# Optimization experiments

Measured on AMD Instinct MI355X. Metric: run time of the kernel, lower is better.

The kernel has to match this reference:

```python
import math
import jax, jax.numpy as jnp
import numpy as np

N = 512
C_S, C_Z, C_H, H, PQ, PV = 384, 128, 16, 12, 4, 8
INF, EPS = 1e5, 1e-8


def _quat_to_rot(q):
    # q: [N,4] unnormalized quaternions -> [N,3,3] rotation matrices
    q = q / jnp.linalg.norm(q, axis=-1, keepdims=True)
    w, x, y, z = q[:, 0], q[:, 1], q[:, 2], q[:, 3]
    return jnp.stack([
        jnp.stack([1 - 2 * (y * y + z * z), 2 * (x * y - w * z), 2 * (x * z + w * y)], -1),
        jnp.stack([2 * (x * y + w * z), 1 - 2 * (x * x + z * z), 2 * (y * z - w * x)], -1),
        jnp.stack([2 * (x * z - w * y), 2 * (y * z + w * x), 1 - 2 * (x * x + y * y)], -1),
    ], -2)


def setup_inputs() -> dict:
    key = jax.random.key(0)
    ks = jax.random.split(key, 16)
    sc = 0.02
    inp = {
        "s": jax.random.normal(ks[0], (N, C_S), jnp.float32),
        "z": jax.random.normal(ks[1], (N, N, C_Z), jnp.float32),
        "rot": _quat_to_rot(jax.random.normal(ks[2], (N, 4), jnp.float32)),
        "trans": jax.random.normal(ks[3], (N, 3), jnp.float32) * 10.0,
        "mask": jnp.ones((N,), jnp.float32),
        "Wq": jax.random.normal(ks[4], (C_S, H * C_H), jnp.float32) * sc,
        "bq": jnp.zeros((H * C_H,), jnp.float32),
        "Wkv": jax.random.normal(ks[5], (C_S, 2 * H * C_H), jnp.float32) * sc,
        "bkv": jnp.zeros((2 * H * C_H,), jnp.float32),
        "Wqp": jax.random.normal(ks[6], (C_S, H * 3 * PQ), jnp.float32) * sc,
        "bqp": jnp.zeros((H * 3 * PQ,), jnp.float32),
        "Wkvp": jax.random.normal(ks[7], (C_S, H * 3 * (PQ + PV)), jnp.float32) * sc,
        "bkvp": jnp.zeros((H * 3 * (PQ + PV),), jnp.float32),
        "Wb": jax.random.normal(ks[8], (C_Z, H), jnp.float32) * sc,
        "bb": jnp.zeros((H,), jnp.float32),
        "head_weights": jnp.full((H,), math.log(math.e - 1.0), jnp.float32),
        "Wout": jax.random.normal(ks[9], (H * (C_Z + C_H + PV * 4), C_S), jnp.float32) * sc,
        "bout": jnp.zeros((C_S,), jnp.float32),
    }
    return inp


def _ipa(s, z, rot, trans, mask, Wq, bq, Wkv, bkv, Wqp, bqp, Wkvp, bkvp, Wb, bb, head_weights, Wout, bout):
    q = (s @ Wq + bq).reshape(N, H, C_H)
    kv = (s @ Wkv + bkv).reshape(N, H, 2 * C_H)
    k, v = kv[..., :C_H], kv[..., C_H:]

    def proj_pts(W, b, P):
        # torch: split last dim into 3 chunks, stack on -1 -> layout [N, 3, H, P] -> [N, H, P, 3]
        pl = (s @ W + b).reshape(N, 3, H, P).transpose(0, 2, 3, 1)
        return jnp.einsum('nij,nhpj->nhpi', rot, pl) + trans[:, None, None, :]

    q_pts = proj_pts(Wqp, bqp, PQ)                    # [N,H,PQ,3]
    kv_pts = proj_pts(Wkvp, bkvp, PQ + PV)            # [N,H,PQ+PV,3]
    k_pts, v_pts = kv_pts[..., :PQ, :], kv_pts[..., PQ:, :]

    b_bias = z @ Wb + bb                              # [N,N,H]
    a = jnp.einsum('ihc,jhc->hij', q, k) * math.sqrt(1.0 / (3 * C_H))
    a = a + math.sqrt(1.0 / 3) * b_bias.transpose(2, 0, 1)

    d2 = jnp.sum((q_pts[:, None] - k_pts[None]) ** 2, axis=-1)   # [i,j,H,PQ]
    hw = jax.nn.softplus(head_weights) * math.sqrt(1.0 / (3 * (PQ * 9.0 / 2)))
    pt_att = -0.5 * jnp.sum(d2 * hw[None, None, :, None], axis=-1)  # [i,j,H]

    sq_mask = INF * (mask[:, None] * mask[None, :] - 1.0)
    a = jax.nn.softmax(a + pt_att.transpose(2, 0, 1) + sq_mask[None], axis=-1)  # [H,i,j]

    o = jnp.einsum('hij,jhc->ihc', a, v).reshape(N, H * C_H)
    o_pt = jnp.einsum('hij,jhpc->ihpc', a, v_pts)                 # [i,H,PV,3]
    o_pt = jnp.einsum('nji,nhpj->nhpi', rot, o_pt - trans[:, None, None, :])  # invert_apply
    o_pt_norm = jnp.sqrt(jnp.sum(o_pt ** 2, axis=-1) + EPS).reshape(N, H * PV)
    o_pt_flat = o_pt.reshape(N, H * PV, 3)
    o_pair = jnp.einsum('hij,ijc->ihc', a, z).reshape(N, H * C_Z)

    cat = jnp.concatenate(
        [o, o_pt_flat[..., 0], o_pt_flat[..., 1], o_pt_flat[..., 2], o_pt_norm, o_pair], axis=-1)
    return cat @ Wout + bout


def reference(s, z, rot, trans, mask, Wq, bq, Wkv, bkv, Wqp, bqp, Wkvp, bkvp, Wb, bb, head_weights, Wout, bout):
    return _ipa(s, z, rot, trans, mask, Wq, bq, Wkv, bkv, Wqp, bqp, Wkvp, bkvp, Wb, bb, head_weights, Wout, bout)
```

## Files before the change

kernel.cpp:

```cpp
#include <hip/hip_runtime.h>
#include <math.h>

#define NN 512
#define CS 384
#define CZ 128
#define CH 16
#define HH 12
#define PQ 4
#define PV 8
#define LGS_S 516

typedef float f32x4 __attribute__((ext_vector_type(4)));
typedef __bf16 bf16x8 __attribute__((ext_vector_type(8)));

__global__ void k_repack(const float* __restrict__ Wq,  const float* __restrict__ bq,
                         const float* __restrict__ Wkv, const float* __restrict__ bkv,
                         const float* __restrict__ Wqp, const float* __restrict__ bqp,
                         const float* __restrict__ Wkvp,const float* __restrict__ bkvp,
                         float* __restrict__ Wcat, float* __restrict__ bcat)
{
    const int total = CS * 1152;
    for (int idx = blockIdx.x * blockDim.x + threadIdx.x; idx < total; idx += gridDim.x * blockDim.x) {
        int kk = idx / 1152, n = idx % 1152;
        float vv;
        if (n < 192)      vv = Wq  [kk * 192 + n];
        else if (n < 576) vv = Wkv [kk * 384 + (n - 192)];
        else if (n < 720) vv = Wqp [kk * 144 + (n - 576)];
        else              vv = Wkvp[kk * 432 + (n - 720)];
        Wcat[idx] = vv;
    }
    int n = blockIdx.x * blockDim.x + threadIdx.x;
    if (n < 1152) {
        float vv;
        if (n < 192)      vv = bq  [n];
        else if (n < 576) vv = bkv [n - 192];
        else if (n < 720) vv = bqp [n - 576];
        else              vv = bkvp[n - 720];
        bcat[n] = vv;
    }
}

__global__ void k_proj(const float* __restrict__ s, const float* __restrict__ Wcat,
                       const float* __restrict__ bcat,
                       float* __restrict__ q, float* __restrict__ k_t, float* __restrict__ v,
                       float* __restrict__ qp_raw, float* __restrict__ kvp_raw)
{
    __shared__ float As[16 * 68];
    __shared__ float Bs[64 * 64];

    int tx = threadIdx.x & 15;
    int ty = threadIdx.x >> 4;
    int n0 = blockIdx.x * 64;
    int m0 = blockIdx.y * 16;

    float acc[4] = {0.f, 0.f, 0.f, 0.f};

    for (int kb = 0; kb < CS; kb += 64) {
        #pragma unroll
        for (int e = 0; e < 4; ++e) {
            int idx = e * 256 + threadIdx.x;
            int m = idx >> 6, kk = idx & 63;
            As[m * 68 + kk] = s[(size_t)(m0 + m) * CS + kb + kk];
        }
        #pragma unroll
        for (int e = 0; e < 16; ++e) {
            int idx = e * 256 + threadIdx.x;
            int kk = idx >> 6, n = idx & 63;
            Bs[kk * 64 + n] = Wcat[(size_t)(kb + kk) * 1152 + n0 + n];
        }
        __syncthreads();

        for (int kk = 0; kk < 64; kk += 4) {
            f32x4 a = *(const f32x4*)&As[ty * 68 + kk];
            f32x4 b[4];
            #pragma unroll
            for (int kq = 0; kq < 4; ++kq)
                b[kq] = *(const f32x4*)&Bs[(kk + kq) * 64 + tx * 4];
            #pragma unroll
            for (int kq = 0; kq < 4; ++kq)
                #pragma unroll
                for (int cc = 0; cc < 4; ++cc)
                    acc[cc] += a[kq] * b[kq][cc];
        }
        __syncthreads();
    }

    int i = m0 + ty;
    #pragma unroll
    for (int cc = 0; cc < 4; ++cc) {
        int col = n0 + tx * 4 + cc;
        float val = acc[cc] + bcat[col];
        if (col < 192) {
            q[i * 192 + col] = val;
        } else if (col < 576) {
            int lc = col - 192;
            int h = lc / 32, w = lc % 32;
            if (w < CH) k_t[(h * CH + w) * NN + i] = val;
            else        v[(i * HH + h) * CH + (w - CH)] = val;
        } else if (col < 720) {
            qp_raw[i * 144 + (col - 576)] = val;
        } else {
            kvp_raw[i * 432 + (col - 720)] = val;
        }
    }
}

__global__ void k_pts_transform(const float* __restrict__ qp_raw, const float* __restrict__ kvp_raw,
                                const float* __restrict__ rot, const float* __restrict__ trans,
                                float* __restrict__ q_pts, float* __restrict__ k_pts_t,
                                float* __restrict__ v_pts)
{
    int idx = blockIdx.x * blockDim.x + threadIdx.x;
    const int total = NN * HH * 16;
    if (idx >= total) return;
    int i = idx / (HH * 16);
    int r = idx % (HH * 16);
    int h = r / 16;
    int p = r % 16;

    float R[9], t3[3];
    for (int a = 0; a < 9; ++a) R[a] = rot[i * 9 + a];
    for (int a = 0; a < 3; ++a) t3[a] = trans[i * 3 + a];

    float x, y, zc;
    if (p < PQ) {
        x  = qp_raw[i * 144 + 0 * 48 + h * PQ + p];
        y  = qp_raw[i * 144 + 1 * 48 + h * PQ + p];
        zc = qp_raw[i * 144 + 2 * 48 + h * PQ + p];
    } else {
        int pp = p - PQ;
        x  = kvp_raw[i * 432 + 0 * 144 + h * 12 + pp];
        y  = kvp_raw[i * 432 + 1 * 144 + h * 12 + pp];
        zc = kvp_raw[i * 432 + 2 * 144 + h * 12 + pp];
    }
    float ox = R[0] * x + R[1] * y + R[2] * zc + t3[0];
    float oy = R[3] * x + R[4] * y + R[5] * zc + t3[1];
    float oz = R[6] * x + R[7] * y + R[8] * zc + t3[2];

    if (p < PQ) {
        int o = ((i * HH + h) * PQ + p) * 3;
        q_pts[o] = ox; q_pts[o + 1] = oy; q_pts[o + 2] = oz;
    } else {
        int pp = p - PQ;
        if (pp < PQ) {
            int rb = (h * PQ + pp) * 3;
            k_pts_t[(size_t)(rb + 0) * NN + i] = ox;
            k_pts_t[(size_t)(rb + 1) * NN + i] = oy;
            k_pts_t[(size_t)(rb + 2) * NN + i] = oz;
        } else {
            int o = ((i * HH + h) * PV + (pp - PQ)) * 3;
            v_pts[o] = ox; v_pts[o + 1] = oy; v_pts[o + 2] = oz;
        }
    }
}

__global__ void __launch_bounds__(512, 4)
k_attn(const float* __restrict__ z, const float* __restrict__ Wb,
       const float* __restrict__ bb,
       const float* __restrict__ q, const float* __restrict__ k_t,
       const float* __restrict__ q_pts, const float* __restrict__ k_pts_t,
       const float* __restrict__ head_weights, const float* __restrict__ mask,
       const float* __restrict__ v, const float* __restrict__ v_pts,
       const float* __restrict__ rot, const float* __restrict__ trans,
       float* __restrict__ cat)
{
    __shared__ float lgs[HH][LGS_S];
    __shared__ float q_lds[HH * CH];
    __shared__ float qp_lds[HH * PQ * 3];
    __shared__ float hw_lds[HH];
    __shared__ float bb_l[HH];
    __shared__ float opt_lds[HH * PV * 3];

    const int i = blockIdx.x;
    const int tid = threadIdx.x;
    const int lane = tid & 63;
    const int wave = tid >> 6;
    const float* zbase = z + (size_t)i * NN * CZ;

    if (tid < HH * CH)     q_lds[tid]  = q[(size_t)i * HH * CH + tid];
    if (tid < HH * PQ * 3) qp_lds[tid] = q_pts[(size_t)i * HH * PQ * 3 + tid];
    if (tid < HH) {
        float x = head_weights[tid];
        hw_lds[tid] = log1pf(expf(x)) * 0.13608276348795434f;
        bb_l[tid] = bb[tid];
    }

    {
        const float b_scale = 0.57735026918962576f;
        const int hcol = lane & 15;
        const int q8 = (lane >> 4) * 8;
        bf16x8 wbf[4];
        #pragma unroll
        for (int kc = 0; kc < 4; ++kc) {
            #pragma unroll
            for (int jj = 0; jj < 8; ++jj) {
                int c = kc * 32 + q8 + jj;
                float wv = (hcol < HH) ? Wb[c * HH + hcol] * b_scale : 0.0f;
                wbf[kc][jj] = (__bf16)wv;
            }
        }
        #pragma unroll
        for (int t = 0; t < 4; ++t) {
            int j0 = (wave * 4 + t) * 16;
            const float* zrow = zbase + (size_t)(j0 + hcol) * CZ;
            f32x4 acc = {0.f, 0.f, 0.f, 0.f};
            #pragma unroll
            for (int kc = 0; kc < 4; ++kc) {
                float4 z0 = *(const float4*)(zrow + kc * 32 + q8);
                float4 z1 = *(const float4*)(zrow + kc * 32 + q8 + 4);
                bf16x8 afrag;
                afrag[0] = (__bf16)z0.x; afrag[1] = (__bf16)z0.y;
                afrag[2] = (__bf16)z0.z; afrag[3] = (__bf16)z0.w;
                afrag[4] = (__bf16)z1.x; afrag[5] = (__bf16)z1.y;
                afrag[6] = (__bf16)z1.z; afrag[7] = (__bf16)z1.w;
                acc = __builtin_amdgcn_mfma_f32_16x16x32_bf16(afrag, wbf[kc], acc, 0, 0, 0);
            }
            if (hcol < HH) {
                #pragma unroll
                for (int r = 0; r < 4; ++r) {
                    int j = j0 + (lane >> 4) * 4 + r;
                    lgs[hcol][j] = acc[r];
                }
            }
        }
    }
    __syncthreads();

    {
        const float qk_scale = 0.14433756729740643f;
        const float b_scale  = 0.57735026918962576f;
        const float sqm = 100000.0f * (mask[i] * mask[tid] - 1.0f);
        #pragma unroll
        for (int h = 0; h < HH; ++h) {
            float accq = 0.f;
            #pragma unroll
            for (int c = 0; c < CH; ++c)
                accq += q_lds[h * CH + c] * k_t[(size_t)(h * CH + c) * NN + tid];
            float s2 = 0.f;
            #pragma unroll
            for (int p = 0; p < PQ; ++p) {
                int rb = (h * PQ + p) * 3;
                float dx = qp_lds[rb + 0] - k_pts_t[(size_t)(rb + 0) * NN + tid];
                float dy = qp_lds[rb + 1] - k_pts_t[(size_t)(rb + 1) * NN + tid];
                float dz = qp_lds[rb + 2] - k_pts_t[(size_t)(rb + 2) * NN + tid];
                s2 += dx * dx + dy * dy + dz * dz;
            }
            lgs[h][tid] += accq * qk_scale + b_scale * bb_l[h] - 0.5f * hw_lds[h] * s2 + sqm;
        }
    }
    __syncthreads();

    for (int row = wave; row < HH; row += 8) {
        float vals[8];
        float m = -1e30f;
        #pragma unroll
        for (int u = 0; u < 8; ++u) { vals[u] = lgs[row][lane + u * 64]; m = fmaxf(m, vals[u]); }
        #pragma unroll
        for (int off = 32; off >= 1; off >>= 1) m = fmaxf(m, __shfl_xor(m, off));
        float ssum = 0.f;
        #pragma unroll
        for (int u = 0; u < 8; ++u) { vals[u] = expf(vals[u] - m); ssum += vals[u]; }
        #pragma unroll
        for (int off = 32; off >= 1; off >>= 1) ssum += __shfl_xor(ssum, off);
        float inv = 1.0f / ssum;
        #pragma unroll
        for (int u = 0; u < 8; ++u) lgs[row][lane + u * 64] = vals[u] * inv;
    }
    __syncthreads();

    if (tid < 480) {
        float acc = 0.f;
        if (tid < 192) {
            const float* lr = lgs[tid >> 4];
            const float* vp = v + tid;
            #pragma unroll 4
            for (int j = 0; j < NN; ++j)
                acc += lr[j] * vp[(size_t)j * 192];
            cat[(size_t)i * 2112 + tid] = acc;
        } else {
            int r = tid - 192;
            const float* lr = lgs[r / 24];
            const float* vp = v_pts + r;
            #pragma unroll 4
            for (int j = 0; j < NN; ++j)
                acc += lr[j] * vp[(size_t)j * 288];
            opt_lds[r] = acc;
        }
    }

    {
        int cl = lane & 15;
        int q4 = lane >> 4;
        int ha = (cl < HH) ? cl : (HH - 1);
        int cb = wave * 16 + cl;
        f32x4 pacc = {0.f, 0.f, 0.f, 0.f};
        for (int ks = 0; ks < 16; ++ks) {
            int jb = ks * 32 + q4 * 8;
            f32x4 a0 = *(const f32x4*)&lgs[ha][jb];
            f32x4 a1 = *(const f32x4*)&lgs[ha][jb + 4];
            bf16x8 af;
            af[0] = (__bf16)a0[0]; af[1] = (__bf16)a0[1];
            af[2] = (__bf16)a0[2]; af[3] = (__bf16)a0[3];
            af[4] = (__bf16)a1[0]; af[5] = (__bf16)a1[1];
            af[6] = (__bf16)a1[2]; af[7] = (__bf16)a1[3];
            bf16x8 bf;
            #pragma unroll
            for (int jj = 0; jj < 8; ++jj)
                bf[jj] = (__bf16)zbase[(size_t)(jb + jj) * CZ + cb];
            pacc = __builtin_amdgcn_mfma_f32_16x16x32_bf16(af, bf, pacc, 0, 0, 0);
        }
        float* crow = cat + (size_t)i * 2112 + 576;
        #pragma unroll
        for (int r = 0; r < 4; ++r) {
            int h = q4 * 4 + r;
            if (h < HH) crow[h * CZ + cb] = pacc[r];
        }
    }
    __syncthreads();

    if (tid < HH * PV) {
        int hp = tid;
        float R[9], t3[3];
        #pragma unroll
        for (int a2 = 0; a2 < 9; ++a2) R[a2] = rot[i * 9 + a2];
        #pragma unroll
        for (int a2 = 0; a2 < 3; ++a2) t3[a2] = trans[i * 3 + a2];
        float gx = opt_lds[hp * 3 + 0] - t3[0];
        float gy = opt_lds[hp * 3 + 1] - t3[1];
        float gz = opt_lds[hp * 3 + 2] - t3[2];
        float lx = R[0] * gx + R[3] * gy + R[6] * gz;
        float ly = R[1] * gx + R[4] * gy + R[7] * gz;
        float lz = R[2] * gx + R[5] * gy + R[8] * gz;
        float* crow = cat + (size_t)i * 2112;
        crow[192 + 0 * 96 + hp] = lx;
        crow[192 + 1 * 96 + hp] = ly;
        crow[192 + 2 * 96 + hp] = lz;
        crow[480 + hp] = sqrtf(lx * lx + ly * ly + lz * lz + 1e-8f);
    }
}

__global__ void k_final(const float* __restrict__ cat, const float* __restrict__ Wout,
                        const float* __restrict__ bout, float* __restrict__ out)
{
    __shared__ float As[16 * 52];
    __shared__ float Bs[48 * 64];

    int tx = threadIdx.x & 15;
    int ty = threadIdx.x >> 4;
    int n0 = blockIdx.x * 64;
    int m0 = blockIdx.y * 16;
    int k0 = blockIdx.z * 528;

    float acc[4] = {0.f, 0.f, 0.f, 0.f};

    for (int stage = 0; stage < 11; ++stage) {
        int kb = k0 + stage * 48;
        #pragma unroll
        for (int e = 0; e < 3; ++e) {
            int idx = e * 256 + threadIdx.x;
            int m = idx / 48, kk = idx % 48;
            As[m * 52 + kk] = cat[(size_t)(m0 + m) * 2112 + kb + kk];
        }
        #pragma unroll
        for (int e = 0; e < 12; ++e) {
            int idx = e * 256 + threadIdx.x;
            int kk = idx >> 6, n = idx & 63;
            Bs[kk * 64 + n] = Wout[(size_t)(kb + kk) * 384 + n0 + n];
        }
        __syncthreads();

        for (int kk = 0; kk < 48; kk += 4) {
            f32x4 a = *(const f32x4*)&As[ty * 52 + kk];
            f32x4 b[4];
            #pragma unroll
            for (int kq = 0; kq < 4; ++kq)
                b[kq] = *(const f32x4*)&Bs[(kk + kq) * 64 + tx * 4];
            #pragma unroll
            for (int kq = 0; kq < 4; ++kq)
                #pragma unroll
                for (int cc = 0; cc < 4; ++cc)
                    acc[cc] += a[kq] * b[kq][cc];
        }
        __syncthreads();
    }

    bool add_bias = (blockIdx.z == 0);
    int m = m0 + ty;
    #pragma unroll
    for (int cc = 0; cc < 4; ++cc) {
        int n = n0 + tx * 4 + cc;
        float val = acc[cc] + (add_bias ? bout[n] : 0.f);
        atomicAdd(&out[(size_t)m * 384 + n], val);
    }
}

extern "C" void kernel_launch(void* const* d_in, const int* in_sizes, int n_in,
                              void* d_out, int out_size, void* d_ws, size_t ws_size,
                              hipStream_t stream)
{
    const float* s     = (const float*)d_in[0];
    const float* z     = (const float*)d_in[1];
    const float* rot   = (const float*)d_in[2];
    const float* trans = (const float*)d_in[3];
    const float* mask  = (const float*)d_in[4];
    const float* Wq    = (const float*)d_in[5];
    const float* bq    = (const float*)d_in[6];
    const float* Wkv   = (const float*)d_in[7];
    const float* bkv   = (const float*)d_in[8];
    const float* Wqp   = (const float*)d_in[9];
    const float* bqp   = (const float*)d_in[10];
    const float* Wkvp  = (const float*)d_in[11];
    const float* bkvp  = (const float*)d_in[12];
    const float* Wb    = (const float*)d_in[13];
    const float* bb    = (const float*)d_in[14];
    const float* hw    = (const float*)d_in[15];
    const float* Wout  = (const float*)d_in[16];
    const float* bout  = (const float*)d_in[17];
    float* out = (float*)d_out;

    float* ws = (float*)d_ws;
    float* q       = ws;
    float* k_t     = ws + 98304;
    float* v       = ws + 196608;
    float* qp_raw  = ws + 294912;
    float* kvp_raw = ws + 368640;
    float* q_pts   = ws + 589824;
    float* k_pts_t = ws + 663552;
    float* v_pts   = ws + 737280;
    float* cat     = ws + 884736;
    float* Wcat    = ws + 1966080;
    float* bcat    = ws + 2408448;

    hipMemsetAsync(out, 0, (size_t)NN * CS * sizeof(float), stream);

    hipLaunchKernelGGL(k_repack, dim3(512), dim3(256), 0, stream,
                       Wq, bq, Wkv, bkv, Wqp, bqp, Wkvp, bkvp, Wcat, bcat);
    hipLaunchKernelGGL(k_proj, dim3(18, 32), dim3(256), 0, stream,
                       s, Wcat, bcat, q, k_t, v, qp_raw, kvp_raw);
    hipLaunchKernelGGL(k_pts_transform, dim3(384), dim3(256), 0, stream,
                       qp_raw, kvp_raw, rot, trans, q_pts, k_pts_t, v_pts);
    hipLaunchKernelGGL(k_attn, dim3(NN), dim3(512), 0, stream,
                       z, Wb, bb, q, k_t, q_pts, k_pts_t, hw, mask,
                       v, v_pts, rot, trans, cat);
    hipLaunchKernelGGL(k_final, dim3(6, 32, 4), dim3(256), 0, stream, cat, Wout, bout, out);
}
```

Baseline: 349.4 us.

## Drop weight repack kernel, hoist logit loads, and split pair-MFMA over K halves

```diff
diff --git a/kernel.cpp b/kernel.cpp
--- a/kernel.cpp
+++ b/kernel.cpp
@@ -13,35 +13,11 @@
 typedef float f32x4 __attribute__((ext_vector_type(4)));
 typedef __bf16 bf16x8 __attribute__((ext_vector_type(8)));
 
-__global__ void k_repack(const float* __restrict__ Wq,  const float* __restrict__ bq,
-                         const float* __restrict__ Wkv, const float* __restrict__ bkv,
-                         const float* __restrict__ Wqp, const float* __restrict__ bqp,
-                         const float* __restrict__ Wkvp,const float* __restrict__ bkvp,
-                         float* __restrict__ Wcat, float* __restrict__ bcat)
-{
-    const int total = CS * 1152;
-    for (int idx = blockIdx.x * blockDim.x + threadIdx.x; idx < total; idx += gridDim.x * blockDim.x) {
-        int kk = idx / 1152, n = idx % 1152;
-        float vv;
-        if (n < 192)      vv = Wq  [kk * 192 + n];
-        else if (n < 576) vv = Wkv [kk * 384 + (n - 192)];
-        else if (n < 720) vv = Wqp [kk * 144 + (n - 576)];
-        else              vv = Wkvp[kk * 432 + (n - 720)];
-        Wcat[idx] = vv;
-    }
-    int n = blockIdx.x * blockDim.x + threadIdx.x;
-    if (n < 1152) {
-        float vv;
-        if (n < 192)      vv = bq  [n];
-        else if (n < 576) vv = bkv [n - 192];
-        else if (n < 720) vv = bqp [n - 576];
-        else              vv = bkvp[n - 720];
-        bcat[n] = vv;
-    }
-}
-
-__global__ void k_proj(const float* __restrict__ s, const float* __restrict__ Wcat,
-                       const float* __restrict__ bcat,
+__global__ void k_proj(const float* __restrict__ s,
+                       const float* __restrict__ Wq,  const float* __restrict__ bq,
+                       const float* __restrict__ Wkv, const float* __restrict__ bkv,
+                       const float* __restrict__ Wqp, const float* __restrict__ bqp,
+                       const float* __restrict__ Wkvp,const float* __restrict__ bkvp,
                        float* __restrict__ q, float* __restrict__ k_t, float* __restrict__ v,
                        float* __restrict__ qp_raw, float* __restrict__ kvp_raw)
 {
@@ -66,7 +42,14 @@
         for (int e = 0; e < 16; ++e) {
             int idx = e * 256 + threadIdx.x;
             int kk = idx >> 6, n = idx & 63;
-            Bs[kk * 64 + n] = Wcat[(size_t)(kb + kk) * 1152 + n0 + n];
+            int col = n0 + n;
+            int kg = kb + kk;
+            float wv;
+            if (col < 192)      wv = Wq  [kg * 192 + col];
+            else if (col < 576) wv = Wkv [kg * 384 + (col - 192)];
+            else if (col < 720) wv = Wqp [kg * 144 + (col - 576)];
+            else                wv = Wkvp[kg * 432 + (col - 720)];
+            Bs[kk * 64 + n] = wv;
         }
         __syncthreads();
 
@@ -89,7 +72,12 @@
     #pragma unroll
     for (int cc = 0; cc < 4; ++cc) {
         int col = n0 + tx * 4 + cc;
-        float val = acc[cc] + bcat[col];
+        float bval;
+        if (col < 192)      bval = bq  [col];
+        else if (col < 576) bval = bkv [col - 192];
+        else if (col < 720) bval = bqp [col - 576];
+        else                bval = bkvp[col - 720];
+        float val = acc[cc] + bval;
         if (col < 192) {
             q[i * 192 + col] = val;
         } else if (col < 576) {
@@ -170,6 +158,7 @@
     __shared__ float hw_lds[HH];
     __shared__ float bb_l[HH];
     __shared__ float opt_lds[HH * PV * 3];
+    __shared__ float pair_lds[HH * CZ];
 
     const int i = blockIdx.x;
     const int tid = threadIdx.x;
@@ -183,6 +172,31 @@
         float x = head_weights[tid];
         hw_lds[tid] = log1pf(expf(x)) * 0.13608276348795434f;
         bb_l[tid] = bb[tid];
+    }
+    __syncthreads();
+
+    float lg[HH];
+    {
+        const float qk_scale = 0.14433756729740643f;
+        const float b_scale  = 0.57735026918962576f;
+        const float sqm = 100000.0f * (mask[i] * mask[tid] - 1.0f);
+        #pragma unroll
+        for (int h = 0; h < HH; ++h) {
+            float accq = 0.f;
+            #pragma unroll
+            for (int c = 0; c < CH; ++c)
+                accq += q_lds[h * CH + c] * k_t[(size_t)(h * CH + c) * NN + tid];
+            float s2 = 0.f;
+            #pragma unroll
+            for (int p = 0; p < PQ; ++p) {
+                int rb = (h * PQ + p) * 3;
+                float dx = qp_lds[rb + 0] - k_pts_t[(size_t)(rb + 0) * NN + tid];
+                float dy = qp_lds[rb + 1] - k_pts_t[(size_t)(rb + 1) * NN + tid];
+                float dz = qp_lds[rb + 2] - k_pts_t[(size_t)(rb + 2) * NN + tid];
+                s2 += dx * dx + dy * dy + dz * dz;
+            }
+            lg[h] = accq * qk_scale + b_scale * bb_l[h] - 0.5f * hw_lds[h] * s2 + sqm;
+        }
     }
 
     {
@@ -224,30 +238,14 @@
             }
         }
     }
-    __syncthreads();
-
-    {
-        const float qk_scale = 0.14433756729740643f;
-        const float b_scale  = 0.57735026918962576f;
-        const float sqm = 100000.0f * (mask[i] * mask[tid] - 1.0f);
-        #pragma unroll
-        for (int h = 0; h < HH; ++h) {
-            float accq = 0.f;
-            #pragma unroll
-            for (int c = 0; c < CH; ++c)
-                accq += q_lds[h * CH + c] * k_t[(size_t)(h * CH + c) * NN + tid];
-            float s2 = 0.f;
-            #pragma unroll
-            for (int p = 0; p < PQ; ++p) {
-                int rb = (h * PQ + p) * 3;
-                float dx = qp_lds[rb + 0] - k_pts_t[(size_t)(rb + 0) * NN + tid];
-                float dy = qp_lds[rb + 1] - k_pts_t[(size_t)(rb + 1) * NN + tid];
-                float dz = qp_lds[rb + 2] - k_pts_t[(size_t)(rb + 2) * NN + tid];
-                s2 += dx * dx + dy * dy + dz * dz;
-            }
-            lgs[h][tid] += accq * qk_scale + b_scale * bb_l[h] - 0.5f * hw_lds[h] * s2 + sqm;
-        }
-    }
+
+    asm volatile("s_waitcnt lgkmcnt(0)" ::: "memory");
+    __builtin_amdgcn_sched_barrier(0);
+
+    #pragma unroll
+    for (int h = 0; h < HH; ++h)
+        lgs[h][tid] += lg[h];
+
     __syncthreads();
 
     for (int row = wave; row < HH; row += 8) {
@@ -273,7 +271,7 @@
         if (tid < 192) {
             const float* lr = lgs[tid >> 4];
             const float* vp = v + tid;
-            #pragma unroll 4
+            #pragma unroll 8
             for (int j = 0; j < NN; ++j)
                 acc += lr[j] * vp[(size_t)j * 192];
             cat[(size_t)i * 2112 + tid] = acc;
@@ -281,21 +279,24 @@
             int r = tid - 192;
             const float* lr = lgs[r / 24];
             const float* vp = v_pts + r;
-            #pragma unroll 4
+            #pragma unroll 8
             for (int j = 0; j < NN; ++j)
                 acc += lr[j] * vp[(size_t)j * 288];
             opt_lds[r] = acc;
         }
     }
 
+    int cl = lane & 15;
+    int q4 = lane >> 4;
+    f32x4 p0 = {0.f, 0.f, 0.f, 0.f};
+    f32x4 p1 = {0.f, 0.f, 0.f, 0.f};
+    const int base = (wave & 3) * 32;
+    const int khalf = wave >> 2;
+    const int c0 = base + 2 * cl;
     {
-        int cl = lane & 15;
-        int q4 = lane >> 4;
         int ha = (cl < HH) ? cl : (HH - 1);
-        int cb = wave * 16 + cl;
-        f32x4 pacc = {0.f, 0.f, 0.f, 0.f};
-        for (int ks = 0; ks < 16; ++ks) {
-            int jb = ks * 32 + q4 * 8;
+        for (int ks8 = 0; ks8 < 8; ++ks8) {
+            int jb = (khalf * 8 + ks8) * 32 + q4 * 8;
             f32x4 a0 = *(const f32x4*)&lgs[ha][jb];
             f32x4 a1 = *(const f32x4*)&lgs[ha][jb + 4];
             bf16x8 af;
@@ -303,20 +304,42 @@
             af[2] = (__bf16)a0[2]; af[3] = (__bf16)a0[3];
             af[4] = (__bf16)a1[0]; af[5] = (__bf16)a1[1];
             af[6] = (__bf16)a1[2]; af[7] = (__bf16)a1[3];
-            bf16x8 bf;
-            #pragma unroll
-            for (int jj = 0; jj < 8; ++jj)
-                bf[jj] = (__bf16)zbase[(size_t)(jb + jj) * CZ + cb];
-            pacc = __builtin_amdgcn_mfma_f32_16x16x32_bf16(af, bf, pacc, 0, 0, 0);
-        }
+            bf16x8 b0, b1;
+            #pragma unroll
+            for (int jj = 0; jj < 8; ++jj) {
+                float2 zz = *(const float2*)&zbase[(size_t)(jb + jj) * CZ + c0];
+                b0[jj] = (__bf16)zz.x;
+                b1[jj] = (__bf16)zz.y;
+            }
+            p0 = __builtin_amdgcn_mfma_f32_16x16x32_bf16(af, b0, p0, 0, 0, 0);
+            p1 = __builtin_amdgcn_mfma_f32_16x16x32_bf16(af, b1, p1, 0, 0, 0);
+        }
+        if (khalf == 0) {
+            #pragma unroll
+            for (int r = 0; r < 4; ++r) {
+                int h = q4 * 4 + r;
+                if (h < HH) {
+                    pair_lds[h * CZ + c0]     = p0[r];
+                    pair_lds[h * CZ + c0 + 1] = p1[r];
+                }
+            }
+        }
+    }
+    __syncthreads();
+
+    if (khalf == 1) {
         float* crow = cat + (size_t)i * 2112 + 576;
         #pragma unroll
         for (int r = 0; r < 4; ++r) {
             int h = q4 * 4 + r;
-            if (h < HH) crow[h * CZ + cb] = pacc[r];
-        }
-    }
-    __syncthreads();
+            if (h < HH) {
+                float2 o2;
+                o2.x = p0[r] + pair_lds[h * CZ + c0];
+                o2.y = p1[r] + pair_lds[h * CZ + c0 + 1];
+                *(float2*)&crow[h * CZ + c0] = o2;
+            }
+        }
+    }
 
     if (tid < HH * PV) {
         int hp = tid;
@@ -428,15 +451,12 @@
     float* k_pts_t = ws + 663552;
     float* v_pts   = ws + 737280;
     float* cat     = ws + 884736;
-    float* Wcat    = ws + 1966080;
-    float* bcat    = ws + 2408448;
 
     hipMemsetAsync(out, 0, (size_t)NN * CS * sizeof(float), stream);
 
-    hipLaunchKernelGGL(k_repack, dim3(512), dim3(256), 0, stream,
-                       Wq, bq, Wkv, bkv, Wqp, bqp, Wkvp, bkvp, Wcat, bcat);
     hipLaunchKernelGGL(k_proj, dim3(18, 32), dim3(256), 0, stream,
-                       s, Wcat, bcat, q, k_t, v, qp_raw, kvp_raw);
+                       s, Wq, bq, Wkv, bkv, Wqp, bqp, Wkvp, bkvp,
+                       q, k_t, v, qp_raw, kvp_raw);
     hipLaunchKernelGGL(k_pts_transform, dim3(384), dim3(256), 0, stream,
                        qp_raw, kvp_raw, rot, trans, q_pts, k_pts_t, v_pts);
     hipLaunchKernelGGL(k_attn, dim3(NN), dim3(512), 0, stream,
```

Result: slower. 868.7 us (+148.6%).
